# Optimization experiments

Measured on AMD Instinct MI355X. Metric: run time of the kernel, lower is better.

Reference implementation:

```python
import jax, jax.numpy as jnp
import numpy as np

N, E, H, D_IN, D_OUT, DEPTH, G = 100000, 1600000, 128, 128, 10, 3, 256


def setup_inputs() -> dict:
    key = jax.random.key(0)
    ks = jax.random.split(key, 16)
    s = lambda k, shape: jax.random.normal(k, shape, dtype=jnp.float32) * 0.05
    inp = {
        "x": jax.random.normal(ks[0], (N, D_IN), dtype=jnp.float32),
        "edge_index": jax.random.randint(ks[1], (2, E), 0, N, dtype=jnp.int32),
        "control_edge_index": jax.random.randint(ks[2], (2, 1024), 0, N, dtype=jnp.int32),
        "batch": jnp.sort(jax.random.randint(ks[3], (N,), 0, G, dtype=jnp.int32)),
        # encoder MLP: input_dim -> hidden -> hidden
        "enc_w1": s(ks[4], (D_IN, H)), "enc_b1": jnp.zeros((H,), jnp.float32),
        "enc_w2": s(ks[5], (H, H)),    "enc_b2": jnp.zeros((H,), jnp.float32),
        # conv_depth GCN layers, hidden -> hidden
        "conv_w": s(ks[6], (DEPTH, H, H)), "conv_b": jnp.zeros((DEPTH, H), jnp.float32),
        # decoder MLP: hidden -> hidden -> output_dim
        "dec_w1": s(ks[7], (H, H)),     "dec_b1": jnp.zeros((H,), jnp.float32),
        "dec_w2": s(ks[8], (H, D_OUT)), "dec_b2": jnp.zeros((D_OUT,), jnp.float32),
    }
    return inp


def _gcn_forward(x, enc_w1, enc_b1, enc_w2, enc_b2, conv_w, conv_b,
                 dec_w1, dec_b1, dec_w2, dec_b2, edge_index, batch):
    # encoder MLP (Linear-ReLU-Dropout(eval)-Linear)
    h = jax.nn.relu(x @ enc_w1 + enc_b1) @ enc_w2 + enc_b2

    # GCN normalization with self-loops: D^{-1/2} (A + I) D^{-1/2}
    loops = jnp.arange(N, dtype=edge_index.dtype)
    src = jnp.concatenate([edge_index[0], loops])  # [E + N]
    dst = jnp.concatenate([edge_index[1], loops])
    deg = jax.ops.segment_sum(jnp.ones_like(src, dtype=h.dtype), dst, num_segments=N)
    inv_sqrt = jax.lax.rsqrt(deg)  # deg >= 1 thanks to self-loops
    coef = (inv_sqrt[src] * inv_sqrt[dst])[:, None]  # [E+N, 1]

    for l in range(DEPTH):
        hw = h @ conv_w[l] + conv_b[l]                      # [N, H]
        h = jax.ops.segment_sum(hw[src] * coef, dst, num_segments=N)
        if l < DEPTH - 1:  # linear=False -> nonlinearity between convs
            h = jax.nn.relu(h)

    # global_add_pool over graph ids
    pooled = jax.ops.segment_sum(h, batch, num_segments=G)   # [G, H]

    # decoder MLP
    return jax.nn.relu(pooled @ dec_w1 + dec_b1) @ dec_w2 + dec_b2  # [G, D_OUT]


def reference(x, edge_index, control_edge_index, batch, enc_w1, enc_b1, enc_w2,
              enc_b2, conv_w, conv_b, dec_w1, dec_b1, dec_w2, dec_b2):
    # control_edge_index corresponds to the (disabled) control mechanism; unused
    return _gcn_forward(x, enc_w1, enc_b1, enc_w2, enc_b2, conv_w, conv_b,
                        dec_w1, dec_b1, dec_w2, dec_b2, edge_index, batch)
```

## Files before the change

kernel.cpp:

```cpp
#include <hip/hip_runtime.h>
#include <hip/hip_bf16.h>
#include <cstdint>
#include <cstddef>

#define NN 100000
#define NE 1600000
#define HH 128
#define NG 256

#define NB 196
#define BSH 9
#define BMSK 511
#define CHUNK 16384
#define NBLK 98

typedef __bf16 bf16x8 __attribute__((ext_vector_type(8)));
typedef float floatx4 __attribute__((ext_vector_type(4)));

__device__ __forceinline__ uint32_t f2b(float f) {
  union { float f; uint32_t u; } v; v.f = f;
  uint32_t u = v.u;
  return (u + 0x7FFFu + ((u >> 16) & 1u)) >> 16;
}
__device__ __forceinline__ float b2f(uint32_t h) {
  union { uint32_t u; float f; } v; v.u = h << 16;
  return v.f;
}
__device__ __forceinline__ void acc8(float* a, uint4 v, float w) {
  a[0] += w * b2f(v.x & 0xFFFFu); a[1] += w * b2f(v.x >> 16);
  a[2] += w * b2f(v.y & 0xFFFFu); a[3] += w * b2f(v.y >> 16);
  a[4] += w * b2f(v.z & 0xFFFFu); a[5] += w * b2f(v.z >> 16);
  a[6] += w * b2f(v.w & 0xFFFFu); a[7] += w * b2f(v.w >> 16);
}


__global__ __launch_bounds__(256) void k_cntA(const int* __restrict__ src,
                                              int* __restrict__ blkcnt) {
  __shared__ int h[NB];
  int t = threadIdx.x;
  if (t < NB) h[t] = 0;
  __syncthreads();
  int base = blockIdx.x * CHUNK, end = min(base + CHUNK, NE);
  for (int i = base + t; i < end; i += 256) atomicAdd(&h[src[i] >> BSH], 1);
  __syncthreads();
  if (t < NB) blkcnt[blockIdx.x * NB + t] = h[t];
}

__global__ __launch_bounds__(256) void k_cntB(const uint2* __restrict__ pairs,
                                              int* __restrict__ blkcnt) {
  __shared__ int h[NB];
  int t = threadIdx.x;
  if (t < NB) h[t] = 0;
  __syncthreads();
  int base = blockIdx.x * CHUNK, end = min(base + CHUNK, NE);
  for (int i = base + t; i < end; i += 256) atomicAdd(&h[pairs[i].y >> BSH], 1);
  __syncthreads();
  if (t < NB) blkcnt[blockIdx.x * NB + t] = h[t];
}

__global__ __launch_bounds__(64) void k_colscan(const int* __restrict__ blkcnt,
                                                int* __restrict__ poff,
                                                int* __restrict__ colsum) {
  int b = blockIdx.x, t = threadIdx.x;
  int carry = 0;
  for (int base = 0; base < NBLK; base += 64) {
    int r = base + t;
    int x = (r < NBLK) ? blkcnt[r * NB + b] : 0;
    int v = x;
    for (int d = 1; d < 64; d <<= 1) { int u = __shfl_up(v, d); if (t >= d) v += u; }
    if (r < NBLK) poff[r * NB + b] = carry + v - x;
    carry += __shfl(v, 63);
  }
  if (t == 0) colsum[b] = carry;
}

__global__ void k_gscan(const int* __restrict__ colsum, int* __restrict__ gbase,
                        int* __restrict__ off, int set_off) {
  __shared__ int s[256];
  int t = threadIdx.x;
  int x = (t < NB) ? colsum[t] : 0;
  s[t] = x; __syncthreads();
  for (int d = 1; d < 256; d <<= 1) {
    int v = (t >= d) ? s[t - d] : 0;
    __syncthreads();
    s[t] += v;
    __syncthreads();
  }
  if (t < NB) gbase[t] = s[t] - x;
  if (t == 0) { gbase[NB] = NE; if (set_off) off[NN] = NE; }
}

__global__ __launch_bounds__(256) void k_placeA(const int* __restrict__ src,
                                                const int* __restrict__ dst,
                                                const int* __restrict__ poff,
                                                const int* __restrict__ gbase,
                                                uint2* __restrict__ pairs) {
  __shared__ int cur[NB];
  int t = threadIdx.x;
  if (t < NB) cur[t] = poff[blockIdx.x * NB + t] + gbase[t];
  __syncthreads();
  int base = blockIdx.x * CHUNK, end = min(base + CHUNK, NE);
  for (int i = base + t; i < end; i += 256) {
    int s = src[i], d = dst[i];
    int p = atomicAdd(&cur[s >> BSH], 1);
    pairs[p] = make_uint2((unsigned)s, (unsigned)d);
  }
}

__global__ __launch_bounds__(256) void k_placeB(const uint2* __restrict__ pairs,
                                                const int* __restrict__ poff,
                                                const int* __restrict__ gbase,
                                                uint32_t* __restrict__ outb) {
  __shared__ int cur[NB];
  int t = threadIdx.x;
  if (t < NB) cur[t] = poff[blockIdx.x * NB + t] + gbase[t];
  __syncthreads();
  int base = blockIdx.x * CHUNK, end = min(base + CHUNK, NE);
  for (int i = base + t; i < end; i += 256) {
    uint2 v = pairs[i];
    int p = atomicAdd(&cur[v.y >> BSH], 1);
    outb[p] = v.x | ((v.y & (unsigned)BMSK) << 17);
  }
}

__global__ __launch_bounds__(256) void k_bucket_sort(
    const uint32_t* __restrict__ pairbuf, const int* __restrict__ gbase,
    int* __restrict__ off, float* __restrict__ inv, int* __restrict__ csrs)
{
  __shared__ int cnt[512];
  __shared__ int loff[512];
  __shared__ int psum[256];
  int b = blockIdx.x;
  int tid = threadIdx.x;
  cnt[tid] = 0; cnt[tid + 256] = 0;
  __syncthreads();
  int s0 = gbase[b], s1 = gbase[b + 1];
  for (int i = s0 + tid; i < s1; i += 256)
    atomicAdd(&cnt[pairbuf[i] >> 17], 1);
  __syncthreads();
  int a0 = cnt[2 * tid], a1 = cnt[2 * tid + 1];
  int s = a0 + a1;
  psum[tid] = s;
  __syncthreads();
  for (int d = 1; d < 256; d <<= 1) {
    int v = (tid >= d) ? psum[tid - d] : 0;
    __syncthreads();
    psum[tid] += v;
    __syncthreads();
  }
  int excl = psum[tid] - s;
  loff[2 * tid] = excl;
  loff[2 * tid + 1] = excl + a0;
  __syncthreads();
#pragma unroll
  for (int k = 0; k < 2; ++k) {
    int i = tid + k * 256;
    int node = b * 512 + i;
    if (node < NN) {
      off[node] = s0 + loff[i];
      inv[node] = rsqrtf((float)cnt[i] + 1.0f);
    }
  }
  __syncthreads();
  cnt[tid] = loff[tid]; cnt[tid + 256] = loff[tid + 256];
  __syncthreads();
  for (int i = s0 + tid; i < s1; i += 256) {
    uint32_t v = pairbuf[i];
    int p = atomicAdd(&cnt[v >> 17], 1);
    csrs[s0 + p] = (int)(v & 0x1FFFFu);
  }
}

__global__ __launch_bounds__(256) void k_deghist(const int* __restrict__ off,
                                                 int* __restrict__ dhist) {
  __shared__ int h[64];
  int t = threadIdx.x;
  if (t < 64) h[t] = 0;
  __syncthreads();
  int i = blockIdx.x * 256 + t;
  if (i < NN) { int d = off[i + 1] - off[i]; if (d > 63) d = 63; atomicAdd(&h[d], 1); }
  __syncthreads();
  if (t < 64 && h[t]) atomicAdd(&dhist[t], h[t]);
}

__global__ void k_dscan(const int* __restrict__ dhist, int* __restrict__ dcur) {
  int t = threadIdx.x;
  int x = dhist[63 - t];
  int v = x;
  for (int d = 1; d < 64; d <<= 1) { int u = __shfl_up(v, d); if (t >= d) v += u; }
  dcur[63 - t] = v - x;
}

__global__ __launch_bounds__(256) void k_dplace(const int* __restrict__ off,
                                                int* __restrict__ dcur,
                                                int* __restrict__ order) {
  __shared__ int h[64], base[64];
  int t = threadIdx.x;
  if (t < 64) h[t] = 0;
  __syncthreads();
  int i = blockIdx.x * 256 + t;
  int d = 0, ld = 0;
  if (i < NN) { d = off[i + 1] - off[i]; if (d > 63) d = 63; ld = atomicAdd(&h[d], 1); }
  __syncthreads();
  if (t < 64) base[t] = h[t] ? atomicAdd(&dcur[t], h[t]) : 0;
  __syncthreads();
  if (i < NN) order[base[d] + ld] = i;
}

__global__ __launch_bounds__(256) void k_gbound(const int* __restrict__ batch,
                                                int* __restrict__ gstart) {
  int i = blockIdx.x * 256 + threadIdx.x;
  if (i >= NN) return;
  int b = batch[i];
  if (i == 0) {
    for (int g = 0; g <= b; ++g) gstart[g] = 0;
  } else {
    int a = batch[i - 1];
    for (int g = a + 1; g <= b; ++g) gstart[g] = i;
  }
  if (i == NN - 1) {
    for (int g = b + 1; g <= NG; ++g) gstart[g] = NN;
  }
}

__global__ __launch_bounds__(256) void k_gemm(
    const uint16_t* __restrict__ A16, const float* __restrict__ A32,
    const float* __restrict__ W, const float* __restrict__ bias,
    uint16_t* __restrict__ Out, int M, int do_relu)
{
  __shared__ uint16_t Wt[128][136];
  const int tid = threadIdx.x;

  for (int it = 0; it < 16; ++it) {
    int idx = tid + it * 256;
    int n = idx & 127;
    int k0 = (idx >> 7) * 4;
    uint2 wv;
    wv.x = f2b(W[(k0 + 0) * 128 + n]) | (f2b(W[(k0 + 1) * 128 + n]) << 16);
    wv.y = f2b(W[(k0 + 2) * 128 + n]) | (f2b(W[(k0 + 3) * 128 + n]) << 16);
    *(uint2*)&Wt[n][k0] = wv;
  }
  __syncthreads();

  const int lane = tid & 63;
  const int wave = tid >> 6;
  const int lrow = lane & 15;
  const int lk = (lane >> 4) * 8;
  const int row0 = blockIdx.x * 128 + wave * 32;

  floatx4 acc[2][8];
#pragma unroll
  for (int t = 0; t < 2; ++t)
#pragma unroll
    for (int n = 0; n < 8; ++n)
      acc[t][n] = (floatx4){0.f, 0.f, 0.f, 0.f};

#pragma unroll
  for (int ks = 0; ks < 4; ++ks) {
    bf16x8 a[2];
#pragma unroll
    for (int t = 0; t < 2; ++t) {
      int r = row0 + t * 16 + lrow;
      uint4 tmp = {0u, 0u, 0u, 0u};
      if (r < M) {
        if (A32) {
          float4 f0 = *(const float4*)(A32 + (size_t)r * HH + ks * 32 + lk);
          float4 f1 = *(const float4*)(A32 + (size_t)r * HH + ks * 32 + lk + 4);
          tmp.x = f2b(f0.x) | (f2b(f0.y) << 16);
          tmp.y = f2b(f0.z) | (f2b(f0.w) << 16);
          tmp.z = f2b(f1.x) | (f2b(f1.y) << 16);
          tmp.w = f2b(f1.z) | (f2b(f1.w) << 16);
        } else {
          tmp = *(const uint4*)(A16 + (size_t)r * HH + ks * 32 + lk);
        }
      }
      a[t] = __builtin_bit_cast(bf16x8, tmp);
    }
#pragma unroll
    for (int n = 0; n < 8; ++n) {
      bf16x8 b = __builtin_bit_cast(bf16x8, *(const uint4*)&Wt[n * 16 + lrow][ks * 32 + lk]);
      acc[0][n] = __builtin_amdgcn_mfma_f32_16x16x32_bf16(a[0], b, acc[0][n], 0, 0, 0);
      acc[1][n] = __builtin_amdgcn_mfma_f32_16x16x32_bf16(a[1], b, acc[1][n], 0, 0, 0);
    }
  }

  float bc[8];
#pragma unroll
  for (int n = 0; n < 8; ++n) bc[n] = bias[n * 16 + lrow];

  const int rbase = (lane >> 4) * 4;
#pragma unroll
  for (int t = 0; t < 2; ++t) {
#pragma unroll
    for (int r = 0; r < 4; ++r) {
      int row = row0 + t * 16 + rbase + r;
      if (row < M) {
#pragma unroll
        for (int n = 0; n < 8; ++n) {
          float v = acc[t][n][r] + bc[n];
          if (do_relu) v = fmaxf(v, 0.f);
          Out[(size_t)row * HH + n * 16 + lrow] = (uint16_t)f2b(v);
        }
      }
    }
  }
}

__global__ __launch_bounds__(256) void k_agg(
    const uint16_t* __restrict__ hw, const int* __restrict__ off,
    const int* __restrict__ csrs, const float* __restrict__ inv,
    const int* __restrict__ order,
    uint16_t* __restrict__ hout, int do_relu)
{
  int slot = blockIdx.x * 16 + (threadIdx.x >> 4);
  if (slot >= NN) return;
  int node = order[slot];
  int c = (threadIdx.x & 15) * 8;

  float invd = inv[node];
  uint4 sv = *(const uint4*)(hw + (size_t)node * HH + c);
  float a[8] = {0.f, 0.f, 0.f, 0.f, 0.f, 0.f, 0.f, 0.f};
  acc8(a, sv, invd);

  int e0 = off[node], e1 = off[node + 1];
  int e = e0;
  for (; e + 4 <= e1; e += 4) {
    int s0 = csrs[e + 0], s1 = csrs[e + 1], s2 = csrs[e + 2], s3 = csrs[e + 3];
    float w0 = inv[s0], w1 = inv[s1], w2 = inv[s2], w3 = inv[s3];
    uint4 v0 = *(const uint4*)(hw + (size_t)s0 * HH + c);
    uint4 v1 = *(const uint4*)(hw + (size_t)s1 * HH + c);
    uint4 v2 = *(const uint4*)(hw + (size_t)s2 * HH + c);
    uint4 v3 = *(const uint4*)(hw + (size_t)s3 * HH + c);
    acc8(a, v0, w0); acc8(a, v1, w1); acc8(a, v2, w2); acc8(a, v3, w3);
  }
  for (; e < e1; ++e) {
    int s = csrs[e];
    float w = inv[s];
    uint4 v = *(const uint4*)(hw + (size_t)s * HH + c);
    acc8(a, v, w);
  }
#pragma unroll
  for (int j = 0; j < 8; ++j) {
    a[j] *= invd;
    if (do_relu) a[j] = fmaxf(a[j], 0.f);
  }
  uint4 o;
  o.x = f2b(a[0]) | (f2b(a[1]) << 16);
  o.y = f2b(a[2]) | (f2b(a[3]) << 16);
  o.z = f2b(a[4]) | (f2b(a[5]) << 16);
  o.w = f2b(a[6]) | (f2b(a[7]) << 16);
  *(uint4*)(hout + (size_t)node * HH + c) = o;
}

__global__ __launch_bounds__(256) void k_pool(const uint16_t* __restrict__ h,
                                              const int* __restrict__ gstart,
                                              float* __restrict__ pooled) {
  __shared__ float red[16][132];
  int g = blockIdx.x;
  int tid = threadIdx.x;
  int slot = tid >> 4;
  int c = (tid & 15) * 8;

  int r0 = gstart[g], r1 = gstart[g + 1];
  float a[8] = {0.f, 0.f, 0.f, 0.f, 0.f, 0.f, 0.f, 0.f};
  for (int r = r0 + slot; r < r1; r += 16) {
    uint4 v = *(const uint4*)(h + (size_t)r * HH + c);
    a[0] += b2f(v.x & 0xFFFFu); a[1] += b2f(v.x >> 16);
    a[2] += b2f(v.y & 0xFFFFu); a[3] += b2f(v.y >> 16);
    a[4] += b2f(v.z & 0xFFFFu); a[5] += b2f(v.z >> 16);
    a[6] += b2f(v.w & 0xFFFFu); a[7] += b2f(v.w >> 16);
  }
  *(float4*)&red[slot][c]     = make_float4(a[0], a[1], a[2], a[3]);
  *(float4*)&red[slot][c + 4] = make_float4(a[4], a[5], a[6], a[7]);
  __syncthreads();
  if (tid < 128) {
    float s = 0.f;
#pragma unroll
    for (int k = 0; k < 16; ++k) s += red[k][tid];
    pooled[g * HH + tid] = s;
  }
}

__global__ void k_dec(const float* __restrict__ pooled,
                      const float* __restrict__ w1, const float* __restrict__ b1,
                      const float* __restrict__ w2, const float* __restrict__ b2,
                      float* __restrict__ out) {
  __shared__ float p[128], t[128];
  int g = blockIdx.x, j = threadIdx.x;
  p[j] = pooled[g * HH + j];
  __syncthreads();
  float a = b1[j];
  for (int k = 0; k < 128; ++k) a += p[k] * w1[k * 128 + j];
  t[j] = fmaxf(a, 0.f);
  __syncthreads();
  if (j < 10) {
    float o = b2[j];
    for (int k = 0; k < 128; ++k) o += t[k] * w2[k * 10 + j];
    out[g * 10 + j] = o;
  }
}

extern "C" void kernel_launch(void* const* d_in, const int* in_sizes, int n_in,
                              void* d_out, int out_size, void* d_ws, size_t ws_size,
                              hipStream_t stream) {
  const float* x       = (const float*)d_in[0];
  const int*   eidx    = (const int*)d_in[1];
  const int*   src     = eidx;
  const int*   dst     = eidx + NE;
  const int*   batch   = (const int*)d_in[3];
  const float* enc_w1  = (const float*)d_in[4];
  const float* enc_b1  = (const float*)d_in[5];
  const float* enc_w2  = (const float*)d_in[6];
  const float* enc_b2  = (const float*)d_in[7];
  const float* conv_w  = (const float*)d_in[8];
  const float* conv_b  = (const float*)d_in[9];
  const float* dec_w1  = (const float*)d_in[10];
  const float* dec_b1  = (const float*)d_in[11];
  const float* dec_w2  = (const float*)d_in[12];
  const float* dec_b2  = (const float*)d_in[13];
  float* out = (float*)d_out;

  char* ws = (char*)d_ws;
  size_t o = 0;
  auto alloc = [&](size_t bytes) -> char* {
    char* p = ws + o;
    o += (bytes + 255) & ~(size_t)255;
    return p;
  };
  int*      off     = (int*)alloc((size_t)(NN + 1) * 4);
  int*      csrs    = (int*)alloc((size_t)NE * 4);
  float*    inv     = (float*)alloc((size_t)NN * 4);
  float*    pooled  = (float*)alloc((size_t)NG * HH * 4);
  int*      blkcntA = (int*)alloc((size_t)NBLK * NB * 4);
  int*      poffA   = (int*)alloc((size_t)NBLK * NB * 4);
  int*      blkcntB = (int*)alloc((size_t)NBLK * NB * 4);
  int*      poffB   = (int*)alloc((size_t)NBLK * NB * 4);
  int*      colsumA = (int*)alloc((size_t)NB * 4);
  int*      colsumB = (int*)alloc((size_t)NB * 4);
  int*      gbaseA  = (int*)alloc((size_t)(NB + 1) * 4);
  int*      gbaseB  = (int*)alloc((size_t)(NB + 1) * 4);
  int*      dhist   = (int*)alloc(64 * 4);
  int*      dcur    = (int*)alloc(64 * 4);
  int*      order   = (int*)alloc((size_t)NN * 4);
  int*      gstart  = (int*)alloc((size_t)(NG + 1) * 4);
  uint16_t* buf0    = (uint16_t*)alloc((size_t)NN * HH * 2);
  uint16_t* buf1    = (uint16_t*)alloc((size_t)NN * HH * 2);
  uint2*    pairsA  = (uint2*)buf1;
  uint32_t* pairB   = (uint32_t*)((char*)buf1 + (size_t)NE * 8);

  hipMemsetAsync(dhist, 0, 64 * 4, stream);

  k_cntA<<<dim3(NBLK), dim3(256), 0, stream>>>(src, blkcntA);
  k_colscan<<<dim3(NB), dim3(64), 0, stream>>>(blkcntA, poffA, colsumA);
  k_gscan<<<dim3(1), dim3(256), 0, stream>>>(colsumA, gbaseA, off, 0);
  k_placeA<<<dim3(NBLK), dim3(256), 0, stream>>>(src, dst, poffA, gbaseA, pairsA);
  k_cntB<<<dim3(NBLK), dim3(256), 0, stream>>>(pairsA, blkcntB);
  k_colscan<<<dim3(NB), dim3(64), 0, stream>>>(blkcntB, poffB, colsumB);
  k_gscan<<<dim3(1), dim3(256), 0, stream>>>(colsumB, gbaseB, off, 1);
  k_placeB<<<dim3(NBLK), dim3(256), 0, stream>>>(pairsA, poffB, gbaseB, pairB);
  k_bucket_sort<<<dim3(NB), dim3(256), 0, stream>>>(pairB, gbaseB, off, inv, csrs);

  const int NBK = (NN + 255) / 256;
  k_deghist<<<dim3(NBK), dim3(256), 0, stream>>>(off, dhist);
  k_dscan<<<dim3(1), dim3(64), 0, stream>>>(dhist, dcur);
  k_dplace<<<dim3(NBK), dim3(256), 0, stream>>>(off, dcur, order);

  k_gbound<<<dim3(NBK), dim3(256), 0, stream>>>(batch, gstart);

  const int GB = (NN + 127) / 128;
  k_gemm<<<dim3(GB), dim3(256), 0, stream>>>(nullptr, x, enc_w1, enc_b1, buf1, NN, 1);
  k_gemm<<<dim3(GB), dim3(256), 0, stream>>>(buf1, nullptr, enc_w2, enc_b2, buf0, NN, 0);

  const int AB = (NN + 15) / 16;
  k_gemm<<<dim3(GB), dim3(256), 0, stream>>>(buf0, nullptr, conv_w + 0 * 16384, conv_b + 0,   buf1, NN, 0);
  k_agg <<<dim3(AB), dim3(256), 0, stream>>>(buf1, off, csrs, inv, order, buf0, 1);
  k_gemm<<<dim3(GB), dim3(256), 0, stream>>>(buf0, nullptr, conv_w + 1 * 16384, conv_b + 128, buf1, NN, 0);
  k_agg <<<dim3(AB), dim3(256), 0, stream>>>(buf1, off, csrs, inv, order, buf0, 1);
  k_gemm<<<dim3(GB), dim3(256), 0, stream>>>(buf0, nullptr, conv_w + 2 * 16384, conv_b + 256, buf1, NN, 0);
  k_agg <<<dim3(AB), dim3(256), 0, stream>>>(buf1, off, csrs, inv, order, buf0, 0);

  k_pool<<<dim3(NG), dim3(256), 0, stream>>>(buf0, gstart, pooled);
  k_dec<<<dim3(NG), dim3(128), 0, stream>>>(pooled, dec_w1, dec_b1, dec_w2, dec_b2, out);
}
```

Measured before the change: 526.6 us.

## Prescale GEMM output by inverse sqrt degree, drop per-edge weight gathers

The GEMM epilogue now multiplies each row by its source node's inverse sqrt degree. The aggregation kernel can then plain-sum neighbour rows and apply the destination scale once, which removes the per-edge gather of inv[src]. The aggregation inner loop is unrolled to 8 neighbours so more loads are in flight, and the degree-histogram and graph-boundary kernels are merged into one launch. Scaling before the bf16 rounding slightly changes the numerics, and the deeper unroll raises register use.

```diff
diff --git a/kernel.cpp b/kernel.cpp
--- a/kernel.cpp
+++ b/kernel.cpp
@@ -26,11 +26,11 @@
   union { uint32_t u; float f; } v; v.u = h << 16;
   return v.f;
 }
-__device__ __forceinline__ void acc8(float* a, uint4 v, float w) {
-  a[0] += w * b2f(v.x & 0xFFFFu); a[1] += w * b2f(v.x >> 16);
-  a[2] += w * b2f(v.y & 0xFFFFu); a[3] += w * b2f(v.y >> 16);
-  a[4] += w * b2f(v.z & 0xFFFFu); a[5] += w * b2f(v.z >> 16);
-  a[6] += w * b2f(v.w & 0xFFFFu); a[7] += w * b2f(v.w >> 16);
+__device__ __forceinline__ void addrow(float* a, uint4 v) {
+  a[0] += b2f(v.x & 0xFFFFu); a[1] += b2f(v.x >> 16);
+  a[2] += b2f(v.y & 0xFFFFu); a[3] += b2f(v.y >> 16);
+  a[4] += b2f(v.z & 0xFFFFu); a[5] += b2f(v.z >> 16);
+  a[6] += b2f(v.w & 0xFFFFu); a[7] += b2f(v.w >> 16);
 }
 
 
@@ -171,14 +171,29 @@
   }
 }
 
-__global__ __launch_bounds__(256) void k_deghist(const int* __restrict__ off,
-                                                 int* __restrict__ dhist) {
+__global__ __launch_bounds__(256) void k_nodeprep(const int* __restrict__ off,
+                                                  const int* __restrict__ batch,
+                                                  int* __restrict__ dhist,
+                                                  int* __restrict__ gstart) {
   __shared__ int h[64];
   int t = threadIdx.x;
   if (t < 64) h[t] = 0;
   __syncthreads();
   int i = blockIdx.x * 256 + t;
-  if (i < NN) { int d = off[i + 1] - off[i]; if (d > 63) d = 63; atomicAdd(&h[d], 1); }
+  if (i < NN) {
+    int d = off[i + 1] - off[i]; if (d > 63) d = 63;
+    atomicAdd(&h[d], 1);
+    int b = batch[i];
+    if (i == 0) {
+      for (int g = 0; g <= b; ++g) gstart[g] = 0;
+    } else {
+      int a = batch[i - 1];
+      for (int g = a + 1; g <= b; ++g) gstart[g] = i;
+    }
+    if (i == NN - 1) {
+      for (int g = b + 1; g <= NG; ++g) gstart[g] = NN;
+    }
+  }
   __syncthreads();
   if (t < 64 && h[t]) atomicAdd(&dhist[t], h[t]);
 }
@@ -207,25 +222,10 @@
   if (i < NN) order[base[d] + ld] = i;
 }
 
-__global__ __launch_bounds__(256) void k_gbound(const int* __restrict__ batch,
-                                                int* __restrict__ gstart) {
-  int i = blockIdx.x * 256 + threadIdx.x;
-  if (i >= NN) return;
-  int b = batch[i];
-  if (i == 0) {
-    for (int g = 0; g <= b; ++g) gstart[g] = 0;
-  } else {
-    int a = batch[i - 1];
-    for (int g = a + 1; g <= b; ++g) gstart[g] = i;
-  }
-  if (i == NN - 1) {
-    for (int g = b + 1; g <= NG; ++g) gstart[g] = NN;
-  }
-}
-
 __global__ __launch_bounds__(256) void k_gemm(
     const uint16_t* __restrict__ A16, const float* __restrict__ A32,
     const float* __restrict__ W, const float* __restrict__ bias,
+    const float* __restrict__ scale,
     uint16_t* __restrict__ Out, int M, int do_relu)
 {
   __shared__ uint16_t Wt[128][136];
@@ -295,10 +295,12 @@
     for (int r = 0; r < 4; ++r) {
       int row = row0 + t * 16 + rbase + r;
       if (row < M) {
+        float sc = scale ? scale[row] : 1.0f;
 #pragma unroll
         for (int n = 0; n < 8; ++n) {
           float v = acc[t][n][r] + bc[n];
           if (do_relu) v = fmaxf(v, 0.f);
+          v *= sc;
           Out[(size_t)row * HH + n * 16 + lrow] = (uint16_t)f2b(v);
         }
       }
@@ -307,7 +309,7 @@
 }
 
 __global__ __launch_bounds__(256) void k_agg(
-    const uint16_t* __restrict__ hw, const int* __restrict__ off,
+    const uint16_t* __restrict__ hw2, const int* __restrict__ off,
     const int* __restrict__ csrs, const float* __restrict__ inv,
     const int* __restrict__ order,
     uint16_t* __restrict__ hout, int do_relu)
@@ -317,28 +319,28 @@
   int node = order[slot];
   int c = (threadIdx.x & 15) * 8;
 
-  float invd = inv[node];
-  uint4 sv = *(const uint4*)(hw + (size_t)node * HH + c);
+  uint4 sv = *(const uint4*)(hw2 + (size_t)node * HH + c);
   float a[8] = {0.f, 0.f, 0.f, 0.f, 0.f, 0.f, 0.f, 0.f};
-  acc8(a, sv, invd);
+  addrow(a, sv);
 
   int e0 = off[node], e1 = off[node + 1];
   int e = e0;
-  for (; e + 4 <= e1; e += 4) {
-    int s0 = csrs[e + 0], s1 = csrs[e + 1], s2 = csrs[e + 2], s3 = csrs[e + 3];
-    float w0 = inv[s0], w1 = inv[s1], w2 = inv[s2], w3 = inv[s3];
-    uint4 v0 = *(const uint4*)(hw + (size_t)s0 * HH + c);
-    uint4 v1 = *(const uint4*)(hw + (size_t)s1 * HH + c);
-    uint4 v2 = *(const uint4*)(hw + (size_t)s2 * HH + c);
-    uint4 v3 = *(const uint4*)(hw + (size_t)s3 * HH + c);
-    acc8(a, v0, w0); acc8(a, v1, w1); acc8(a, v2, w2); acc8(a, v3, w3);
+  for (; e + 8 <= e1; e += 8) {
+    int s[8];
+#pragma unroll
+    for (int k = 0; k < 8; ++k) s[k] = csrs[e + k];
+    uint4 v[8];
+#pragma unroll
+    for (int k = 0; k < 8; ++k) v[k] = *(const uint4*)(hw2 + (size_t)s[k] * HH + c);
+#pragma unroll
+    for (int k = 0; k < 8; ++k) addrow(a, v[k]);
   }
   for (; e < e1; ++e) {
     int s = csrs[e];
-    float w = inv[s];
-    uint4 v = *(const uint4*)(hw + (size_t)s * HH + c);
-    acc8(a, v, w);
-  }
+    uint4 v = *(const uint4*)(hw2 + (size_t)s * HH + c);
+    addrow(a, v);
+  }
+  float invd = inv[node];
 #pragma unroll
   for (int j = 0; j < 8; ++j) {
     a[j] *= invd;
@@ -461,22 +463,20 @@
   k_bucket_sort<<<dim3(NB), dim3(256), 0, stream>>>(pairB, gbaseB, off, inv, csrs);
 
   const int NBK = (NN + 255) / 256;
-  k_deghist<<<dim3(NBK), dim3(256), 0, stream>>>(off, dhist);
+  k_nodeprep<<<dim3(NBK), dim3(256), 0, stream>>>(off, batch, dhist, gstart);
   k_dscan<<<dim3(1), dim3(64), 0, stream>>>(dhist, dcur);
   k_dplace<<<dim3(NBK), dim3(256), 0, stream>>>(off, dcur, order);
 
-  k_gbound<<<dim3(NBK), dim3(256), 0, stream>>>(batch, gstart);
-
   const int GB = (NN + 127) / 128;
-  k_gemm<<<dim3(GB), dim3(256), 0, stream>>>(nullptr, x, enc_w1, enc_b1, buf1, NN, 1);
-  k_gemm<<<dim3(GB), dim3(256), 0, stream>>>(buf1, nullptr, enc_w2, enc_b2, buf0, NN, 0);
+  k_gemm<<<dim3(GB), dim3(256), 0, stream>>>(nullptr, x, enc_w1, enc_b1, nullptr, buf1, NN, 1);
+  k_gemm<<<dim3(GB), dim3(256), 0, stream>>>(buf1, nullptr, enc_w2, enc_b2, nullptr, buf0, NN, 0);
 
   const int AB = (NN + 15) / 16;
-  k_gemm<<<dim3(GB), dim3(256), 0, stream>>>(buf0, nullptr, conv_w + 0 * 16384, conv_b + 0,   buf1, NN, 0);
+  k_gemm<<<dim3(GB), dim3(256), 0, stream>>>(buf0, nullptr, conv_w + 0 * 16384, conv_b + 0,   inv, buf1, NN, 0);
   k_agg <<<dim3(AB), dim3(256), 0, stream>>>(buf1, off, csrs, inv, order, buf0, 1);
-  k_gemm<<<dim3(GB), dim3(256), 0, stream>>>(buf0, nullptr, conv_w + 1 * 16384, conv_b + 128, buf1, NN, 0);
+  k_gemm<<<dim3(GB), dim3(256), 0, stream>>>(buf0, nullptr, conv_w + 1 * 16384, conv_b + 128, inv, buf1, NN, 0);
   k_agg <<<dim3(AB), dim3(256), 0, stream>>>(buf1, off, csrs, inv, order, buf0, 1);
-  k_gemm<<<dim3(GB), dim3(256), 0, stream>>>(buf0, nullptr, conv_w + 2 * 16384, conv_b + 256, buf1, NN, 0);
+  k_gemm<<<dim3(GB), dim3(256), 0, stream>>>(buf0, nullptr, conv_w + 2 * 16384, conv_b + 256, inv, buf1, NN, 0);
   k_agg <<<dim3(AB), dim3(256), 0, stream>>>(buf1, off, csrs, inv, order, buf0, 0);
 
   k_pool<<<dim3(NG), dim3(256), 0, stream>>>(buf0, gstart, pooled);
```

Result: slower. 537.9 us (+2.1%).
